# Optimization experiments

Measured on AMD Instinct MI355X. Metric: run time of the kernel, lower is better.

The kernel has to match this reference:

```python
import jax, jax.numpy as jnp
import numpy as np

EMB = 512
N_LAYERS = 8
N_HEADS = 16
FF_MULT = 4
NUM_PATCHES = 196
B = 32
N_VIS = 49
LN_EPS = 1e-5


def _sincos_1d(embed_dim, pos):
    omega = np.arange(embed_dim // 2, dtype=np.float64)
    omega /= embed_dim / 2.0
    omega = 1.0 / 10000 ** omega
    pos = pos.reshape(-1)
    out = np.einsum('m,d->md', pos, omega)
    return np.concatenate([np.sin(out), np.cos(out)], axis=1)


def _sincos_2d(embed_dim, grid_size):
    grid_h = np.arange(grid_size, dtype=np.float32)
    grid_w = np.arange(grid_size, dtype=np.float32)
    grid = np.stack(np.meshgrid(grid_w, grid_h), axis=0).reshape([2, 1, grid_size, grid_size])
    emb_h = _sincos_1d(embed_dim // 2, grid[0])
    emb_w = _sincos_1d(embed_dim // 2, grid[1])
    return np.concatenate([emb_h, emb_w], axis=1)


def setup_inputs() -> dict:
    key = jax.random.key(0)
    ks = jax.random.split(key, 20)
    D, H, FF, L = EMB, N_HEADS, FF_MULT * EMB, N_LAYERS
    s = 0.02
    inp = {}
    inp['x_enc_out_vis'] = jax.random.normal(ks[0], (B, N_VIS + 1, D), dtype=jnp.float32)
    # per-batch permutation of [0, NUM_PATCHES)
    u = jax.random.uniform(ks[1], (B, NUM_PATCHES))
    inp['idx_restore_patches'] = jnp.argsort(u, axis=1).astype(jnp.int32)
    inp['mask_token'] = jax.random.normal(ks[2], (1, 1, D), dtype=jnp.float32) * s
    inp['pos_emb'] = jnp.asarray(_sincos_2d(D, int(NUM_PATCHES ** 0.5))[None], dtype=jnp.float32)
    # stacked per-layer params, layout [in, out] (equivalent to torch Linear math)
    inp['Wq'] = jax.random.normal(ks[3], (L, D, D), dtype=jnp.float32) * s
    inp['bq'] = jnp.zeros((L, D), jnp.float32)
    inp['Wk'] = jax.random.normal(ks[4], (L, D, D), dtype=jnp.float32) * s
    inp['bk'] = jnp.zeros((L, D), jnp.float32)
    inp['Wv'] = jax.random.normal(ks[5], (L, D, D), dtype=jnp.float32) * s
    inp['bv'] = jnp.zeros((L, D), jnp.float32)
    inp['Wo'] = jax.random.normal(ks[6], (L, D, D), dtype=jnp.float32) * s
    inp['bo'] = jnp.zeros((L, D), jnp.float32)
    inp['ln1_g'] = jnp.ones((L, D), jnp.float32)
    inp['ln1_b'] = jnp.zeros((L, D), jnp.float32)
    inp['W1'] = jax.random.normal(ks[7], (L, D, FF), dtype=jnp.float32) * s
    inp['b1'] = jnp.zeros((L, FF), jnp.float32)
    inp['W2'] = jax.random.normal(ks[8], (L, FF, D), dtype=jnp.float32) * s
    inp['b2'] = jnp.zeros((L, D), jnp.float32)
    inp['ln2_g'] = jnp.ones((L, D), jnp.float32)
    inp['ln2_b'] = jnp.zeros((L, D), jnp.float32)
    inp['lnf_g'] = jnp.ones((D,), jnp.float32)
    inp['lnf_b'] = jnp.zeros((D,), jnp.float32)
    return inp


def _layernorm(x, g, b):
    m = jnp.mean(x, axis=-1, keepdims=True)
    v = jnp.mean((x - m) ** 2, axis=-1, keepdims=True)
    return (x - m) * jax.lax.rsqrt(v + LN_EPS) * g + b


def _decoder_forward(x_enc_out_vis, idx_restore, mask_token, pos_emb,
                     Wq, bq, Wk, bk, Wv, bv, Wo, bo, ln1_g, ln1_b,
                     W1, b1, W2, b2, ln2_g, ln2_b, lnf_g, lnf_b):
    Bsz, Nvis1, D = x_enc_out_vis.shape
    N = pos_emb.shape[1]
    H = N_HEADS
    hd = D // H
    # reassemble: visible patches (drop CLS) followed by mask tokens, then unshuffle
    vis = x_enc_out_vis[:, 1:]                                   # [B, Nvis, D]
    mtok = jnp.broadcast_to(mask_token, (Bsz, N - (Nvis1 - 1), D))
    shuffled = jnp.concatenate([vis, mtok], axis=1)              # [B, N, D]
    x = jnp.take_along_axis(shuffled, idx_restore[:, :, None], axis=1) + pos_emb

    def block(x, p):
        wq, bq_, wk, bk_, wv, bv_, wo, bo_, g1, be1, w1, bf1, w2, bf2, g2, be2 = p
        q = (x @ wq + bq_).reshape(Bsz, N, H, hd).transpose(0, 2, 1, 3)
        k = (x @ wk + bk_).reshape(Bsz, N, H, hd).transpose(0, 2, 1, 3)
        v = (x @ wv + bv_).reshape(Bsz, N, H, hd).transpose(0, 2, 1, 3)
        scores = jnp.einsum('bhqd,bhkd->bhqk', q, k) / jnp.sqrt(jnp.float32(hd))
        attn = jax.nn.softmax(scores, axis=-1)
        o = jnp.einsum('bhqk,bhkd->bhqd', attn, v)
        o = o.transpose(0, 2, 1, 3).reshape(Bsz, N, D)
        attended = o @ wo + bo_
        x = _layernorm(attended + x, g1, be1)
        ff = jax.nn.relu(x @ w1 + bf1) @ w2 + bf2
        x = _layernorm(ff + x, g2, be2)
        return x, None

    params = (Wq, bq, Wk, bk, Wv, bv, Wo, bo, ln1_g, ln1_b, W1, b1, W2, b2, ln2_g, ln2_b)
    x, _ = jax.lax.scan(block, x, params)
    return _layernorm(x, lnf_g, lnf_b)


def reference(x_enc_out_vis, idx_restore_patches, mask_token, pos_emb,
              Wq, bq, Wk, bk, Wv, bv, Wo, bo, ln1_g, ln1_b,
              W1, b1, W2, b2, ln2_g, ln2_b, lnf_g, lnf_b):
    return _decoder_forward(x_enc_out_vis, idx_restore_patches, mask_token, pos_emb,
                            Wq, bq, Wk, bk, Wv, bv, Wo, bo, ln1_g, ln1_b,
                            W1, b1, W2, b2, ln2_g, ln2_b, lnf_g, lnf_b)
```

## Files before the change

kernel.cpp:

```cpp
#include <hip/hip_runtime.h>

#define LAYERS 8
#define DIM 512
#define FFD 2048
#define NTOK 6272
#define NSEQ 196
#define BATCH 32
#define NHEAD 16
#define HD 32
#define NP 224

typedef unsigned short u16;
typedef __bf16 bf16x8 __attribute__((ext_vector_type(8)));
typedef float f32x4 __attribute__((ext_vector_type(4)));
typedef unsigned short u16x8 __attribute__((ext_vector_type(8)));

__device__ __forceinline__ u16 f2bf(float f) {
    unsigned u = __float_as_uint(f);
    u += 0x7FFF + ((u >> 16) & 1);
    return (u16)(u >> 16);
}
__device__ __forceinline__ float bf2f(u16 u) {
    return __uint_as_float((unsigned)u << 16);
}

typedef __attribute__((address_space(1))) void gvoid_t;
typedef __attribute__((address_space(3))) void lvoid_t;
__device__ __forceinline__ void gload_lds16(const void* g, void* l) {
    __builtin_amdgcn_global_load_lds((gvoid_t*)g, (lvoid_t*)l, 16, 0, 0);
}

__global__ __launch_bounds__(256) void transpose_w4(const float* __restrict__ Wq,
                                                    const float* __restrict__ Wk,
                                                    const float* __restrict__ Wv,
                                                    const float* __restrict__ Wo,
                                                    u16* __restrict__ out) {
    __shared__ float t[32][33];
    int z = blockIdx.z;
    int sel = z >> 3, l = z & 7;
    const float* in = (sel == 0) ? Wq : (sel == 1) ? Wk : (sel == 2) ? Wv : Wo;
    size_t ibase = (size_t)l * DIM * DIM;
    size_t obase = (size_t)z * DIM * DIM;
    int n0 = blockIdx.x * 32, k0 = blockIdx.y * 32;
    int tx = threadIdx.x, ty = threadIdx.y;
#pragma unroll
    for (int i = 0; i < 4; ++i)
        t[ty + i * 8][tx] = in[ibase + (size_t)(k0 + ty + i * 8) * DIM + n0 + tx];
    __syncthreads();
#pragma unroll
    for (int i = 0; i < 4; ++i)
        out[obase + (size_t)(n0 + ty + i * 8) * DIM + k0 + tx] = f2bf(t[tx][ty + i * 8]);
}

__global__ __launch_bounds__(256) void transpose_w(const float* __restrict__ in,
                                                   u16* __restrict__ out, int K, int N) {
    __shared__ float t[32][33];
    size_t base = (size_t)blockIdx.z * K * N;
    int n0 = blockIdx.x * 32, k0 = blockIdx.y * 32;
    int tx = threadIdx.x, ty = threadIdx.y;
#pragma unroll
    for (int i = 0; i < 4; ++i)
        t[ty + i * 8][tx] = in[base + (size_t)(k0 + ty + i * 8) * N + n0 + tx];
    __syncthreads();
#pragma unroll
    for (int i = 0; i < 4; ++i)
        out[base + (size_t)(n0 + ty + i * 8) * K + k0 + tx] = f2bf(t[tx][ty + i * 8]);
}

__global__ void pack3_bias(const float* __restrict__ a, const float* __restrict__ b,
                           const float* __restrict__ c, float* __restrict__ o, int n) {
    int i = blockIdx.x * 256 + threadIdx.x;
    if (i < n) { o[i] = a[i]; o[n + i] = b[i]; o[2 * n + i] = c[i]; }
}

__global__ __launch_bounds__(128) void gather_pos(const float* __restrict__ xenc,
                                                  const int* __restrict__ idx,
                                                  const float* __restrict__ mtok,
                                                  const float* __restrict__ pos,
                                                  float* __restrict__ x, u16* __restrict__ xb) {
    int token = blockIdx.x;
    int b = token / NSEQ, t = token - b * NSEQ;
    int id = idx[token];
    const float* src = (id < 49) ? (xenc + ((size_t)b * 50 + id + 1) * DIM) : mtok;
    int d = threadIdx.x * 4;
    float4 s = *(const float4*)(src + d);
    float4 p = *(const float4*)(pos + (size_t)t * DIM + d);
    float4 r;
    r.x = s.x + p.x; r.y = s.y + p.y; r.z = s.z + p.z; r.w = s.w + p.w;
    *(float4*)(x + (size_t)token * DIM + d) = r;
    ushort4 rb;
    rb.x = f2bf(r.x); rb.y = f2bf(r.y); rb.z = f2bf(r.z); rb.w = f2bf(r.w);
    *(ushort4*)(xb + (size_t)token * DIM + d) = rb;
}

template<int EPI>
__global__ __launch_bounds__(256) void gemm4(
    const u16* __restrict__ A, int lda, long long zsA,
    const u16* __restrict__ Bt, int ldb, long long zsB,
    const float* __restrict__ bias, long long zsBias,
    u16* __restrict__ outB, long long zsOut,
    int N, int K) {
    __shared__ u16 As[2][128 * 64];
    __shared__ u16 Bs[2][128 * 64];
    int tid = threadIdx.x;
    int lane = tid & 63, wid = tid >> 6;
    int z = blockIdx.z;
    const u16* Az = A + (size_t)z * zsA;
    const u16* Bz = Bt + (size_t)z * zsB;
    int m0 = blockIdx.y * 128, n0 = blockIdx.x * 128;
    int l16 = lane & 15, kq = lane >> 4;
    int wm = (wid >> 1) * 64, wn = (wid & 1) * 64;

    f32x4 acc[4][4];
    f32x4 zero = {0.f, 0.f, 0.f, 0.f};
#pragma unroll
    for (int a = 0; a < 4; ++a)
#pragma unroll
        for (int b = 0; b < 4; ++b) acc[a][b] = zero;

#define STAGE(buf, kk)                                                             \
    {                                                                              \
        _Pragma("unroll")                                                          \
        for (int i_ = 0; i_ < 4; ++i_) {                                           \
            int c_ = i_ * 256 + tid;                     \
            int row_ = c_ >> 3;                           \
            int kof_ = ((c_ & 7) * 16) ^ ((row_ & 7) << 4);                        \
            gload_lds16((const char*)Az + ((size_t)(m0 + row_) * lda + (kk)) * 2 + kof_, \
                        (char*)As[buf] + (size_t)c_ * 16);                         \
            gload_lds16((const char*)Bz + ((size_t)(n0 + row_) * ldb + (kk)) * 2 + kof_, \
                        (char*)Bs[buf] + (size_t)c_ * 16);                         \
        }                                                                          \
    }

    int nk = K >> 6;
    STAGE(0, 0);
    for (int kt = 0; kt < nk; ++kt) {
        int cur = kt & 1;
        if (kt + 1 < nk) {
            STAGE(cur ^ 1, (kt + 1) << 6);
            asm volatile("s_waitcnt vmcnt(8)" ::: "memory");
        } else {
            asm volatile("s_waitcnt vmcnt(0)" ::: "memory");
        }
        __builtin_amdgcn_s_barrier();
        const char* Ac = (const char*)As[cur];
        const char* Bc = (const char*)Bs[cur];
#pragma unroll
        for (int kh = 0; kh < 2; ++kh) {
            bf16x8 af[4], bfr[4];
#pragma unroll
            for (int mr = 0; mr < 4; ++mr) {
                int row = wm + mr * 16 + l16;
                int cb = (kh * 64 + kq * 16) ^ ((row & 7) << 4);
                af[mr] = *(const bf16x8*)(Ac + row * 128 + cb);
            }
#pragma unroll
            for (int nc = 0; nc < 4; ++nc) {
                int row = wn + nc * 16 + l16;
                int cb = (kh * 64 + kq * 16) ^ ((row & 7) << 4);
                bfr[nc] = *(const bf16x8*)(Bc + row * 128 + cb);
            }
#pragma unroll
            for (int mr = 0; mr < 4; ++mr)
#pragma unroll
                for (int nc = 0; nc < 4; ++nc)
                    acc[mr][nc] = __builtin_amdgcn_mfma_f32_16x16x32_bf16(af[mr], bfr[nc],
                                                                          acc[mr][nc], 0, 0, 0);
        }
        __builtin_amdgcn_s_barrier();
    }
#undef STAGE

    const float* biasz = (EPI != 4) ? bias + (size_t)z * zsBias : nullptr;
#pragma unroll
    for (int mr = 0; mr < 4; ++mr)
#pragma unroll
        for (int nc = 0; nc < 4; ++nc)
#pragma unroll
            for (int i = 0; i < 4; ++i) {
                int rg = m0 + wm + mr * 16 + kq * 4 + i;
                int cg = n0 + wn + nc * 16 + l16;
                float v = acc[mr][nc][i];
                size_t off = (size_t)z * zsOut + (size_t)rg * N + cg;
                if (EPI == 1) { v += biasz[cg]; outB[off] = f2bf(v > 0.f ? v : 0.f); }
                else if (EPI == 3) { v += biasz[cg]; outB[off] = f2bf(v); }
                else outB[off] = f2bf(v);
            }
}

__global__ __launch_bounds__(256) void red_ln(const u16* __restrict__ p0, long long ps,
                                              const float* __restrict__ bias,
                                              const float* __restrict__ gg,
                                              const float* __restrict__ bb,
                                              float* __restrict__ x, u16* __restrict__ xb) {
    int t = blockIdx.x * 4 + (threadIdx.x >> 6);
    int lane = threadIdx.x & 63;
    size_t base = (size_t)t * DIM;
    int c0 = lane * 8;
    u16x8 pa = *(const u16x8*)(p0 + base + c0);
    u16x8 pb = *(const u16x8*)(p0 + ps + base + c0);
    float4 xa = *(const float4*)(x + base + c0);
    float4 xc = *(const float4*)(x + base + c0 + 4);
    float4 ba = *(const float4*)(bias + c0);
    float4 bc = *(const float4*)(bias + c0 + 4);
    float xs[8] = {xa.x, xa.y, xa.z, xa.w, xc.x, xc.y, xc.z, xc.w};
    float bs[8] = {ba.x, ba.y, ba.z, ba.w, bc.x, bc.y, bc.z, bc.w};
    float v[8];
    float s = 0.f, s2 = 0.f;
#pragma unroll
    for (int i = 0; i < 8; ++i) {
        v[i] = bf2f(pa[i]) + bf2f(pb[i]) + bs[i] + xs[i];
        s += v[i]; s2 += v[i] * v[i];
    }
#pragma unroll
    for (int off = 32; off; off >>= 1) { s += __shfl_xor(s, off); s2 += __shfl_xor(s2, off); }
    float m = s * (1.f / 512.f);
    float var = s2 * (1.f / 512.f) - m * m;
    float rs = rsqrtf(var + 1e-5f);
    float4 ga = *(const float4*)(gg + c0);
    float4 gc = *(const float4*)(gg + c0 + 4);
    float4 b0 = *(const float4*)(bb + c0);
    float4 b1 = *(const float4*)(bb + c0 + 4);
    float gs[8] = {ga.x, ga.y, ga.z, ga.w, gc.x, gc.y, gc.z, gc.w};
    float os[8] = {b0.x, b0.y, b0.z, b0.w, b1.x, b1.y, b1.z, b1.w};
    float o[8];
    u16x8 ob16;
#pragma unroll
    for (int i = 0; i < 8; ++i) {
        o[i] = (v[i] - m) * rs * gs[i] + os[i];
        ob16[i] = f2bf(o[i]);
    }
    float4 o0 = {o[0], o[1], o[2], o[3]};
    float4 o1 = {o[4], o[5], o[6], o[7]};
    *(float4*)(x + base + c0) = o0;
    *(float4*)(x + base + c0 + 4) = o1;
    *(u16x8*)(xb + base + c0) = ob16;
}

__global__ __launch_bounds__(256) void attn_mfma(const u16* __restrict__ qkvb,
                                                 u16* __restrict__ ob) {
    __shared__ u16 Ks[NP * 32];
    __shared__ u16 VTs[32 * 232];
    __shared__ u16 Ps[4][16 * 128];
    int bh = blockIdx.x >> 1, half = blockIdx.x & 1;
    int b = bh >> 4, h = bh & 15;
    int tid = threadIdx.x, lane = tid & 63, wid = tid >> 6;
    int l16 = lane & 15, kq = lane >> 4;
    const size_t MS = (size_t)NTOK * DIM;
    const u16* qg = qkvb + ((size_t)b * NSEQ) * DIM + h * HD;
    const u16* kg = qg + MS;
    const u16* vg = qg + 2 * MS;

    for (int c = tid; c < 784; c += 256) {
        int row = c >> 2, ch = c & 3;
        gload_lds16(kg + (size_t)row * DIM + ch * 8, (char*)Ks + c * 16);
    }
    for (int i = tid; i < 448; i += 256) ((unsigned*)(Ks + 196 * 32))[i] = 0;
    for (int i = tid; i < 1568; i += 256) {
        int j = i >> 3, d0 = (i & 7) * 4;
        ushort4 vv = *(const ushort4*)(vg + (size_t)j * DIM + d0);
        VTs[(d0 + 0) * 232 + j] = vv.x;
        VTs[(d0 + 1) * 232 + j] = vv.y;
        VTs[(d0 + 2) * 232 + j] = vv.z;
        VTs[(d0 + 3) * 232 + j] = vv.w;
    }
    for (int i = tid; i < 1024; i += 256) {
        int d = i >> 5, j = 196 + (i & 31);
        VTs[d * 232 + j] = 0;
    }
    __syncthreads();

    const float scale = 0.17677669529663687f;
    char* psb = (char*)&Ps[wid][0];
    int pend = half ? 13 : 7;

    for (int p = half * 7 + wid; p < pend; p += 4) {
        int r0 = p * 16;
        int qrow = r0 + l16; if (qrow > 195) qrow = 195;
        bf16x8 qf = *(const bf16x8*)(qg + (size_t)qrow * DIM + kq * 8);

        f32x4 z4 = {0.f, 0.f, 0.f, 0.f};
        f32x4 s[14];
#pragma unroll
        for (int ct = 0; ct < 14; ++ct) {
            bf16x8 kf = *(const bf16x8*)&Ks[(ct * 16 + l16) * 32 + kq * 8];
            s[ct] = __builtin_amdgcn_mfma_f32_16x16x32_bf16(qf, kf, z4, 0, 0, 0);
        }
        bool v12 = (l16 < 4);
        float mx[4], sum[4], inv[4];
#pragma unroll
        for (int i = 0; i < 4; ++i) {
            float m = -1e30f;
#pragma unroll
            for (int ct = 0; ct < 12; ++ct) m = fmaxf(m, s[ct][i]);
            if (v12) m = fmaxf(m, s[12][i]);
            mx[i] = m * scale;
        }
#pragma unroll
        for (int off = 8; off; off >>= 1)
#pragma unroll
            for (int i = 0; i < 4; ++i) mx[i] = fmaxf(mx[i], __shfl_xor(mx[i], off));
#pragma unroll
        for (int i = 0; i < 4; ++i) sum[i] = 0.f;
#pragma unroll
        for (int ct = 0; ct < 14; ++ct)
#pragma unroll
            for (int i = 0; i < 4; ++i) {
                bool valid = (ct < 12) || (ct == 12 && v12);
                float e = valid ? __expf(s[ct][i] * scale - mx[i]) : 0.f;
                s[ct][i] = e;
                sum[i] += e;
            }
#pragma unroll
        for (int off = 8; off; off >>= 1)
#pragma unroll
            for (int i = 0; i < 4; ++i) sum[i] += __shfl_xor(sum[i], off);
#pragma unroll
        for (int i = 0; i < 4; ++i) inv[i] = 1.f / sum[i];

        f32x4 o0 = {0.f, 0.f, 0.f, 0.f}, o1 = {0.f, 0.f, 0.f, 0.f};
#pragma unroll
        for (int ct = 0; ct < 8; ++ct)
#pragma unroll
            for (int i = 0; i < 4; ++i) {
                int rl = kq * 4 + i;
                int byte = rl * 256 + (((ct * 16 + l16) * 2) ^ ((rl & 7) << 4));
                *(u16*)(psb + byte) = f2bf(s[ct][i]);
            }
#pragma unroll
        for (int kt = 0; kt < 4; ++kt) {
            int K2 = (kt * 64 + kq * 16) ^ ((l16 & 7) << 4);
            bf16x8 pa = *(const bf16x8*)(psb + l16 * 256 + K2);
            bf16x8 va = *(const bf16x8*)&VTs[l16 * 232 + kt * 32 + kq * 8];
            bf16x8 vb = *(const bf16x8*)&VTs[(16 + l16) * 232 + kt * 32 + kq * 8];
            o0 = __builtin_amdgcn_mfma_f32_16x16x32_bf16(pa, va, o0, 0, 0, 0);
            o1 = __builtin_amdgcn_mfma_f32_16x16x32_bf16(pa, vb, o1, 0, 0, 0);
        }
#pragma unroll
        for (int ct = 8; ct < 14; ++ct)
#pragma unroll
            for (int i = 0; i < 4; ++i) {
                int rl = kq * 4 + i;
                int byte = rl * 256 + ((((ct - 8) * 16 + l16) * 2) ^ ((rl & 7) << 4));
                *(u16*)(psb + byte) = f2bf(s[ct][i]);
            }
#pragma unroll
        for (int kt = 4; kt < 7; ++kt) {
            int K2 = ((kt - 4) * 64 + kq * 16) ^ ((l16 & 7) << 4);
            bf16x8 pa = *(const bf16x8*)(psb + l16 * 256 + K2);
            bf16x8 va = *(const bf16x8*)&VTs[l16 * 232 + kt * 32 + kq * 8];
            bf16x8 vb = *(const bf16x8*)&VTs[(16 + l16) * 232 + kt * 32 + kq * 8];
            o0 = __builtin_amdgcn_mfma_f32_16x16x32_bf16(pa, va, o0, 0, 0, 0);
            o1 = __builtin_amdgcn_mfma_f32_16x16x32_bf16(pa, vb, o1, 0, 0, 0);
        }
#pragma unroll
        for (int i = 0; i < 4; ++i) {
            int row = r0 + kq * 4 + i;
            if (row < NSEQ) {
                size_t rb = ((size_t)b * NSEQ + row) * DIM + h * HD;
                ob[rb + l16] = f2bf(o0[i] * inv[i]);
                ob[rb + 16 + l16] = f2bf(o1[i] * inv[i]);
            }
        }
    }
}

__global__ __launch_bounds__(256) void ln_final(const float* __restrict__ y,
                                                const float* __restrict__ gg,
                                                const float* __restrict__ bb,
                                                float* __restrict__ xout) {
    int t = blockIdx.x * 4 + (threadIdx.x >> 6);
    int lane = threadIdx.x & 63;
    const float* row = y + (size_t)t * DIM;
    float4 a = *(const float4*)(row + lane * 4);
    float4 c = *(const float4*)(row + 256 + lane * 4);
    float s = a.x + a.y + a.z + a.w + c.x + c.y + c.z + c.w;
    float s2 = a.x * a.x + a.y * a.y + a.z * a.z + a.w * a.w
             + c.x * c.x + c.y * c.y + c.z * c.z + c.w * c.w;
#pragma unroll
    for (int off = 32; off; off >>= 1) { s += __shfl_xor(s, off); s2 += __shfl_xor(s2, off); }
    float m = s * (1.f / 512.f);
    float var = s2 * (1.f / 512.f) - m * m;
    float rs = rsqrtf(var + 1e-5f);
    float4 g0 = *(const float4*)(gg + lane * 4);
    float4 g1 = *(const float4*)(gg + 256 + lane * 4);
    float4 b0 = *(const float4*)(bb + lane * 4);
    float4 b1 = *(const float4*)(bb + 256 + lane * 4);
    float4 o0, o1;
    o0.x = (a.x - m) * rs * g0.x + b0.x;
    o0.y = (a.y - m) * rs * g0.y + b0.y;
    o0.z = (a.z - m) * rs * g0.z + b0.z;
    o0.w = (a.w - m) * rs * g0.w + b0.w;
    o1.x = (c.x - m) * rs * g1.x + b1.x;
    o1.y = (c.y - m) * rs * g1.y + b1.y;
    o1.z = (c.z - m) * rs * g1.z + b1.z;
    o1.w = (c.w - m) * rs * g1.w + b1.w;
    *(float4*)(xout + (size_t)t * DIM + lane * 4) = o0;
    *(float4*)(xout + (size_t)t * DIM + 256 + lane * 4) = o1;
}

extern "C" void kernel_launch(void* const* d_in, const int* in_sizes, int n_in,
                              void* d_out, int out_size, void* d_ws, size_t ws_size,
                              hipStream_t stream) {
    const float* xenc = (const float*)d_in[0];
    const int*   idxr = (const int*)d_in[1];
    const float* mtok = (const float*)d_in[2];
    const float* pos  = (const float*)d_in[3];
    const float* Wq = (const float*)d_in[4];  const float* bq = (const float*)d_in[5];
    const float* Wk = (const float*)d_in[6];  const float* bk = (const float*)d_in[7];
    const float* Wv = (const float*)d_in[8];  const float* bv = (const float*)d_in[9];
    const float* Wo = (const float*)d_in[10]; const float* bo = (const float*)d_in[11];
    const float* ln1g = (const float*)d_in[12]; const float* ln1b = (const float*)d_in[13];
    const float* W1 = (const float*)d_in[14]; const float* b1 = (const float*)d_in[15];
    const float* W2 = (const float*)d_in[16]; const float* b2 = (const float*)d_in[17];
    const float* ln2g = (const float*)d_in[18]; const float* ln2b = (const float*)d_in[19];
    const float* lnfg = (const float*)d_in[20]; const float* lnfb = (const float*)d_in[21];

    char* w = (char*)d_ws;
    u16* WTqkvo = (u16*)w; w += (size_t)4 * LAYERS * DIM * DIM * 2;
    u16* WT1    = (u16*)w; w += (size_t)LAYERS * DIM * FFD * 2;
    u16* WT2    = (u16*)w; w += (size_t)LAYERS * FFD * DIM * 2;
    float* bqkv = (float*)w; w += (size_t)3 * LAYERS * DIM * 4;
    float* x    = (float*)w; w += (size_t)NTOK * DIM * 4;
    u16*   xb   = (u16*)w;  w += (size_t)NTOK * DIM * 2;
    u16*   qkvb = (u16*)w;  w += (size_t)3 * NTOK * DIM * 2;
    u16*   ob   = (u16*)w;  w += (size_t)NTOK * DIM * 2;
    u16*   hb   = (u16*)w;  w += (size_t)NTOK * FFD * 2;
    size_t need = (size_t)(w - (char*)d_ws);
    if (ws_size < need) return;

    u16* pp = qkvb;
    const long long ND = (long long)NTOK * DIM;

    const size_t WL = (size_t)DIM * DIM;

    transpose_w4<<<dim3(DIM / 32, DIM / 32, 4 * LAYERS), dim3(32, 8), 0, stream>>>(Wq, Wk, Wv, Wo, WTqkvo);
    transpose_w<<<dim3(FFD / 32, DIM / 32, LAYERS), dim3(32, 8), 0, stream>>>(W1, WT1, DIM, FFD);
    transpose_w<<<dim3(DIM / 32, FFD / 32, LAYERS), dim3(32, 8), 0, stream>>>(W2, WT2, FFD, DIM);
    pack3_bias<<<(LAYERS * DIM + 255) / 256, 256, 0, stream>>>(bq, bk, bv, bqkv, LAYERS * DIM);

    gather_pos<<<NTOK, 128, 0, stream>>>(xenc, idxr, mtok, pos, x, xb);

    for (int l = 0; l < LAYERS; ++l) {
        gemm4<3><<<dim3(4, 49, 3), 256, 0, stream>>>(
            xb, DIM, 0, WTqkvo + l * WL, DIM, (long long)LAYERS * WL,
            bqkv + l * DIM, (long long)LAYERS * DIM,
            qkvb, ND, DIM, DIM);
        attn_mfma<<<BATCH * NHEAD * 2, 256, 0, stream>>>(qkvb, ob);
        gemm4<4><<<dim3(4, 49, 2), 256, 0, stream>>>(
            ob, DIM, 256, WTqkvo + 3 * (size_t)LAYERS * WL + l * WL, DIM, 256,
            nullptr, 0, pp, ND, DIM, 256);
        red_ln<<<NTOK / 4, 256, 0, stream>>>(pp, ND, bo + l * DIM,
                                             ln1g + l * DIM, ln1b + l * DIM, x, xb);
        gemm4<1><<<dim3(16, 49, 1), 256, 0, stream>>>(
            xb, DIM, 0, WT1 + (size_t)l * DIM * FFD, DIM, 0,
            b1 + l * FFD, 0, hb, 0, FFD, DIM);
        gemm4<4><<<dim3(4, 49, 2), 256, 0, stream>>>(
            hb, FFD, 1024, WT2 + (size_t)l * FFD * DIM, FFD, 1024,
            nullptr, 0, pp, ND, DIM, 1024);
        red_ln<<<NTOK / 4, 256, 0, stream>>>(pp, ND, b2 + l * DIM,
                                             ln2g + l * DIM, ln2b + l * DIM, x, xb);
    }
    ln_final<<<NTOK / 4, 256, 0, stream>>>(x, lnfg, lnfb, (float*)d_out);
}
```

Before: 983.5 us.

## Remap GEMM blocks XCD-aware, split FF2 K four ways, prioritize attention MFMA

GEMM launches become 1D grids, and each workgroup index is remapped so that consecutive logical M tiles land on the same XCD, which should improve L2 reuse of shared B/A tiles. The second FFN GEMM now splits K into four 512-wide slices instead of two, raising the block count to 784 for better CU fill. red_ln is templated on the number of partial sums so it can reduce four slices. Attention wraps its MFMA sections in s_setprio hints to favor matrix issue. The extra split adds partial-sum traffic and reduction work.

```diff
diff --git a/kernel.cpp b/kernel.cpp
--- a/kernel.cpp
+++ b/kernel.cpp
@@ -99,15 +99,24 @@
     const u16* __restrict__ Bt, int ldb, long long zsB,
     const float* __restrict__ bias, long long zsBias,
     u16* __restrict__ outB, long long zsOut,
-    int N, int K) {
+    int N, int K, int nN, int nM) {
     __shared__ u16 As[2][128 * 64];
     __shared__ u16 Bs[2][128 * 64];
     int tid = threadIdx.x;
     int lane = tid & 63, wid = tid >> 6;
-    int z = blockIdx.z;
+
+    int nwg = gridDim.x;
+    int q8 = nwg >> 3, r8 = nwg & 7;
+    int xcd = blockIdx.x & 7, slot = blockIdx.x >> 3;
+    int w = (xcd < r8 ? xcd * (q8 + 1) : r8 * (q8 + 1) + (xcd - r8) * q8) + slot;
+    int m = w % nM;
+    int nz = w / nM;
+    int n = nz % nN;
+    int z = nz / nN;
+
     const u16* Az = A + (size_t)z * zsA;
     const u16* Bz = Bt + (size_t)z * zsB;
-    int m0 = blockIdx.y * 128, n0 = blockIdx.x * 128;
+    int m0 = m * 128, n0 = n * 128;
     int l16 = lane & 15, kq = lane >> 4;
     int wm = (wid >> 1) * 64, wn = (wid & 1) * 64;
 
@@ -188,6 +197,7 @@
             }
 }
 
+template<int NS>
 __global__ __launch_bounds__(256) void red_ln(const u16* __restrict__ p0, long long ps,
                                               const float* __restrict__ bias,
                                               const float* __restrict__ gg,
@@ -197,19 +207,28 @@
     int lane = threadIdx.x & 63;
     size_t base = (size_t)t * DIM;
     int c0 = lane * 8;
-    u16x8 pa = *(const u16x8*)(p0 + base + c0);
-    u16x8 pb = *(const u16x8*)(p0 + ps + base + c0);
+    float v[8];
+    {
+        u16x8 pa = *(const u16x8*)(p0 + base + c0);
+#pragma unroll
+        for (int i = 0; i < 8; ++i) v[i] = bf2f(pa[i]);
+    }
+#pragma unroll
+    for (int s2i = 1; s2i < NS; ++s2i) {
+        u16x8 pb = *(const u16x8*)(p0 + (size_t)s2i * ps + base + c0);
+#pragma unroll
+        for (int i = 0; i < 8; ++i) v[i] += bf2f(pb[i]);
+    }
     float4 xa = *(const float4*)(x + base + c0);
     float4 xc = *(const float4*)(x + base + c0 + 4);
     float4 ba = *(const float4*)(bias + c0);
     float4 bc = *(const float4*)(bias + c0 + 4);
     float xs[8] = {xa.x, xa.y, xa.z, xa.w, xc.x, xc.y, xc.z, xc.w};
     float bs[8] = {ba.x, ba.y, ba.z, ba.w, bc.x, bc.y, bc.z, bc.w};
-    float v[8];
     float s = 0.f, s2 = 0.f;
 #pragma unroll
     for (int i = 0; i < 8; ++i) {
-        v[i] = bf2f(pa[i]) + bf2f(pb[i]) + bs[i] + xs[i];
+        v[i] += bs[i] + xs[i];
         s += v[i]; s2 += v[i] * v[i];
     }
 #pragma unroll
@@ -281,11 +300,13 @@
 
         f32x4 z4 = {0.f, 0.f, 0.f, 0.f};
         f32x4 s[14];
+        __builtin_amdgcn_s_setprio(1);
 #pragma unroll
         for (int ct = 0; ct < 14; ++ct) {
             bf16x8 kf = *(const bf16x8*)&Ks[(ct * 16 + l16) * 32 + kq * 8];
             s[ct] = __builtin_amdgcn_mfma_f32_16x16x32_bf16(qf, kf, z4, 0, 0, 0);
         }
+        __builtin_amdgcn_s_setprio(0);
         bool v12 = (l16 < 4);
         float mx[4], sum[4], inv[4];
 #pragma unroll
@@ -327,6 +348,7 @@
                 int byte = rl * 256 + (((ct * 16 + l16) * 2) ^ ((rl & 7) << 4));
                 *(u16*)(psb + byte) = f2bf(s[ct][i]);
             }
+        __builtin_amdgcn_s_setprio(1);
 #pragma unroll
         for (int kt = 0; kt < 4; ++kt) {
             int K2 = (kt * 64 + kq * 16) ^ ((l16 & 7) << 4);
@@ -336,6 +358,7 @@
             o0 = __builtin_amdgcn_mfma_f32_16x16x32_bf16(pa, va, o0, 0, 0, 0);
             o1 = __builtin_amdgcn_mfma_f32_16x16x32_bf16(pa, vb, o1, 0, 0, 0);
         }
+        __builtin_amdgcn_s_setprio(0);
 #pragma unroll
         for (int ct = 8; ct < 14; ++ct)
 #pragma unroll
@@ -344,6 +367,7 @@
                 int byte = rl * 256 + ((((ct - 8) * 16 + l16) * 2) ^ ((rl & 7) << 4));
                 *(u16*)(psb + byte) = f2bf(s[ct][i]);
             }
+        __builtin_amdgcn_s_setprio(1);
 #pragma unroll
         for (int kt = 4; kt < 7; ++kt) {
             int K2 = ((kt - 4) * 64 + kq * 16) ^ ((l16 & 7) << 4);
@@ -353,6 +377,7 @@
             o0 = __builtin_amdgcn_mfma_f32_16x16x32_bf16(pa, va, o0, 0, 0, 0);
             o1 = __builtin_amdgcn_mfma_f32_16x16x32_bf16(pa, vb, o1, 0, 0, 0);
         }
+        __builtin_amdgcn_s_setprio(0);
 #pragma unroll
         for (int i = 0; i < 4; ++i) {
             int row = r0 + kq * 4 + i;
@@ -442,24 +467,24 @@
     gather_pos<<<NTOK, 128, 0, stream>>>(xenc, idxr, mtok, pos, x, xb);
 
     for (int l = 0; l < LAYERS; ++l) {
-        gemm4<3><<<dim3(4, 49, 3), 256, 0, stream>>>(
+        gemm4<3><<<588, 256, 0, stream>>>(
             xb, DIM, 0, WTqkvo + l * WL, DIM, (long long)LAYERS * WL,
             bqkv + l * DIM, (long long)LAYERS * DIM,
-            qkvb, ND, DIM, DIM);
+            qkvb, ND, DIM, DIM, 4, 49);
         attn_mfma<<<BATCH * NHEAD * 2, 256, 0, stream>>>(qkvb, ob);
-        gemm4<4><<<dim3(4, 49, 2), 256, 0, stream>>>(
+        gemm4<4><<<392, 256, 0, stream>>>(
             ob, DIM, 256, WTqkvo + 3 * (size_t)LAYERS * WL + l * WL, DIM, 256,
-            nullptr, 0, pp, ND, DIM, 256);
-        red_ln<<<NTOK / 4, 256, 0, stream>>>(pp, ND, bo + l * DIM,
-                                             ln1g + l * DIM, ln1b + l * DIM, x, xb);
-        gemm4<1><<<dim3(16, 49, 1), 256, 0, stream>>>(
+            nullptr, 0, pp, ND, DIM, 256, 4, 49);
+        red_ln<2><<<NTOK / 4, 256, 0, stream>>>(pp, ND, bo + l * DIM,
+                                                ln1g + l * DIM, ln1b + l * DIM, x, xb);
+        gemm4<1><<<784, 256, 0, stream>>>(
             xb, DIM, 0, WT1 + (size_t)l * DIM * FFD, DIM, 0,
-            b1 + l * FFD, 0, hb, 0, FFD, DIM);
-        gemm4<4><<<dim3(4, 49, 2), 256, 0, stream>>>(
-            hb, FFD, 1024, WT2 + (size_t)l * FFD * DIM, FFD, 1024,
-            nullptr, 0, pp, ND, DIM, 1024);
-        red_ln<<<NTOK / 4, 256, 0, stream>>>(pp, ND, b2 + l * DIM,
-                                             ln2g + l * DIM, ln2b + l * DIM, x, xb);
+            b1 + l * FFD, 0, hb, 0, FFD, DIM, 16, 49);
+        gemm4<4><<<784, 256, 0, stream>>>(
+            hb, FFD, 512, WT2 + (size_t)l * FFD * DIM, FFD, 512,
+            nullptr, 0, pp, ND, DIM, 512, 4, 49);
+        red_ln<4><<<NTOK / 4, 256, 0, stream>>>(pp, ND, b2 + l * DIM,
+                                                ln2g + l * DIM, ln2b + l * DIM, x, xb);
     }
     ln_final<<<NTOK / 4, 256, 0, stream>>>(x, lnfg, lnfb, (float*)d_out);
 }
```

After: 1.049 ms. +6.7%, slower.
